# Performance work log

Hardware: AMD Instinct MI355X
Metric: run time of the kernel (lower is better)

The kernel has to match this reference:

```python
import jax, jax.numpy as jnp
import numpy as np
from jax import lax

K_NEIGHBORS = 50
KERNEL_DELTA = 1e-3


def _predict(x, w1, b1, w2, b2, w3, b3):
    # valuePredictor: Linear(512,256)-ELU-Linear(256,128)-ELU-Linear(128,5)
    h = jax.nn.elu(x @ w1 + b1)
    h = jax.nn.elu(h @ w2 + b2)
    p = h @ w3 + b3  # [B, 2 + action_space]
    value = p[:, 0]
    done = jax.nn.sigmoid(p[:, 1])
    logits = p[:, 2:]
    return value, done, logits


def _dnd_lookup(q, mem_keys, mem_vals, act):
    # q: [B, D]; mem_keys/mem_vals: [A, N, D]; act: [B] bank indices.
    # NEC-style DND: top-k nearest keys, inverse-distance kernel weighted value sum.
    B, D = q.shape
    A, N, _ = mem_keys.shape
    qn = jnp.sum(q * q, axis=-1)                      # [B]
    kn = jnp.sum(mem_keys * mem_keys, axis=-1)        # [A, N]
    dot = jnp.einsum('bd,and->ban', q, mem_keys)      # [B, A, N]
    dist = qn[:, None, None] + kn[None] - 2.0 * dot   # squared L2, [B, A, N]
    neg_d, idx = lax.top_k(-dist, K_NEIGHBORS)        # [B, A, K]
    d = -neg_d
    w = 1.0 / (d + KERNEL_DELTA)
    w = w / jnp.sum(w, axis=-1, keepdims=True)        # [B, A, K]
    vals_b = jnp.broadcast_to(mem_vals[None], (B, A, N, D))
    gathered = jnp.take_along_axis(vals_b, idx[..., None], axis=2)  # [B, A, K, D]
    out_all = jnp.sum(w[..., None] * gathered, axis=2)              # [B, A, D]
    return out_all[jnp.arange(B), act]                              # [B, D]


def setup_inputs() -> dict:
    key = jax.random.key(0)
    ks = jax.random.split(key, 8)
    B, D, A, N = 256, 512, 3, 25000
    x = jax.random.normal(ks[0], (B, D), dtype=jnp.float32)
    actions = jax.random.randint(ks[1], (B, 5), 0, A, dtype=jnp.int32)
    mem_keys = jax.random.normal(ks[2], (A, N, D), dtype=jnp.float32)
    mem_vals = jax.random.normal(ks[3], (A, N, D), dtype=jnp.float32)
    w1 = jax.random.normal(ks[4], (D, 256), dtype=jnp.float32) * (1.0 / np.sqrt(D))
    b1 = jnp.zeros((256,), jnp.float32)
    w2 = jax.random.normal(ks[5], (256, 128), dtype=jnp.float32) * (1.0 / np.sqrt(256))
    b2 = jnp.zeros((128,), jnp.float32)
    w3 = jax.random.normal(ks[6], (128, 5), dtype=jnp.float32) * (1.0 / np.sqrt(128))
    b3 = jnp.zeros((5,), jnp.float32)
    return {"x": x, "actions": actions, "mem_keys": mem_keys, "mem_vals": mem_vals,
            "w1": w1, "b1": b1, "w2": w2, "b2": b2, "w3": w3, "b3": b3}


def reference(x, actions, mem_keys, mem_vals, w1, b1, w2, b2, w3, b3):
    # Batched version of the per-sample loop: step-0 prediction on the
    # embedding, then 5 chained DND lookups each followed by a prediction.
    values, dones, logits = [], [], []
    v, dn, lg = _predict(x, w1, b1, w2, b2, w3, b3)
    values.append(v); dones.append(dn); logits.append(lg)
    emb = x
    for j in range(5):
        emb = _dnd_lookup(emb, mem_keys, mem_vals, actions[:, j])
        v, dn, lg = _predict(emb, w1, b1, w2, b2, w3, b3)
        values.append(v); dones.append(dn); logits.append(lg)
    values = jnp.stack(values, axis=1)   # [B, 6]
    dones = jnp.stack(dones, axis=1)     # [B, 6]
    logits = jnp.stack(logits, axis=1)   # [B, 6, 3]
    # pack into a single tensor [B, 6, 5]: (value, done, 3 action logits)
    return jnp.concatenate([values[..., None], dones[..., None], logits], axis=-1)
```

## Files before the change

### kernel.cpp

```cpp
#include <hip/hip_runtime.h>

#define BATCH 256
#define DIM 512
#define NACT 3
#define NMEM 25000
#define KNB 50
#define H1N 256
#define H2N 128
#define NSTEPS 5
#define KDELTA 0.001f

#define TB 128
#define TN 64
#define BK 64
#define NCH (DIM / BK)
#define NYT ((NMEM + TN - 1) / TN)

#define CAP 2048
#define MAXPT 12
#define ZTHR 2.40f

typedef __attribute__((ext_vector_type(8))) short short8;
typedef __attribute__((ext_vector_type(4))) float f32x4;

__device__ __forceinline__ unsigned short bf16rn(float f) {
    unsigned u = __float_as_uint(f);
    u += 0x7FFFu + ((u >> 16) & 1u);
    return (unsigned short)(u >> 16);
}
__device__ __forceinline__ float blo(unsigned u) { return __uint_as_float(u << 16); }
__device__ __forceinline__ float bhi(unsigned u) { return __uint_as_float(u & 0xFFFF0000u); }

__global__ __launch_bounds__(256)
void prep_keys_kernel(const float* __restrict__ rows, unsigned short* __restrict__ kb,
                      float* __restrict__ kn, int nrows) {
    int wave = threadIdx.x >> 6, lane = threadIdx.x & 63;
    int r = blockIdx.x * 4 + wave;
    if (r >= nrows) return;
    const float* p = rows + (size_t)r * DIM;
    float4 v0 = *(const float4*)(p + lane * 8);
    float4 v1 = *(const float4*)(p + lane * 8 + 4);
    float f[8] = {v0.x, v0.y, v0.z, v0.w, v1.x, v1.y, v1.z, v1.w};
    short8 hv;
    float s = 0.f;
    #pragma unroll
    for (int i = 0; i < 8; ++i) { hv[i] = (short)bf16rn(f[i]); s += f[i] * f[i]; }
    *(short8*)(kb + (size_t)r * DIM + lane * 8) = hv;
    for (int off = 32; off; off >>= 1) s += __shfl_down(s, off);
    if (lane == 0) kn[r] = s;
}

__global__ __launch_bounds__(256)
void knstats_kernel(const float* __restrict__ kn, float* __restrict__ knm,
                    float* __restrict__ knv) {
    int a = blockIdx.x, tid = threadIdx.x;
    __shared__ float ss[256], qq[256];
    float s = 0.f, q = 0.f;
    for (int i = tid; i < NMEM; i += 256) {
        float v = kn[a * NMEM + i];
        s += v; q += v * v;
    }
    ss[tid] = s; qq[tid] = q;
    __syncthreads();
    for (int st = 128; st > 0; st >>= 1) {
        if (tid < st) { ss[tid] += ss[tid + st]; qq[tid] += qq[tid + st]; }
        __syncthreads();
    }
    if (tid == 0) {
        float mean = ss[0] / (float)NMEM;
        knm[a] = mean;
        knv[a] = fmaxf(qq[0] / (float)NMEM - mean * mean, 0.f);
    }
}

__global__ __launch_bounds__(256)
void group_all_kernel(const int* __restrict__ actions,
                      int* __restrict__ perm, int* __restrict__ cnt) {
    int step = blockIdx.x;
    __shared__ int lcnt[NACT];
    __shared__ int lperm[NACT * BATCH];
    int tid = threadIdx.x;
    if (tid < NACT) lcnt[tid] = 0;
    __syncthreads();
    int a = actions[tid * NSTEPS + step];
    int pos = atomicAdd(&lcnt[a], 1);
    lperm[a * BATCH + pos] = tid;
    __syncthreads();
    if (tid < NACT) cnt[step * 4 + tid] = lcnt[tid];
    for (int aa = 0; aa < NACT; ++aa) {
        int c = lcnt[aa];
        int f = (c > 0) ? lperm[aa * BATCH] : 0;
        for (int i = c + tid; i < BATCH; i += 256) lperm[aa * BATCH + i] = f;
    }
    __syncthreads();
    for (int i = tid; i < NACT * BATCH; i += 256)
        perm[step * NACT * BATCH + i] = lperm[i];
}

__global__ __launch_bounds__(256)
void prep_predict_kernel(const float* __restrict__ x, unsigned short* __restrict__ eb,
                         float* __restrict__ qn, const int* __restrict__ actions,
                         const float* __restrict__ knm, const float* __restrict__ knv,
                         float* __restrict__ Tb, float* __restrict__ sw,
                         const float* __restrict__ w1, const float* __restrict__ b1,
                         const float* __restrict__ w2, const float* __restrict__ b2,
                         const float* __restrict__ w3, const float* __restrict__ b3,
                         float* __restrict__ out) {
    int b = blockIdx.x, tid = threadIdx.x;
    __shared__ float xs[DIM];
    __shared__ float red[256];
    __shared__ float h1[H1N];
    __shared__ float h2[H2N];
    float e0 = x[(size_t)b * DIM + tid];
    float e1 = x[(size_t)b * DIM + tid + 256];
    xs[tid] = e0; xs[tid + 256] = e1;
    eb[(size_t)b * DIM + tid] = bf16rn(e0);
    eb[(size_t)b * DIM + tid + 256] = bf16rn(e1);
    red[tid] = e0 * e0 + e1 * e1;
    __syncthreads();
    for (int s = 128; s > 0; s >>= 1) { if (tid < s) red[tid] += red[tid + s]; __syncthreads(); }
    if (tid == 0) {
        float q = red[0];
        qn[b] = q;
        int a0 = actions[b * NSTEPS];
        float s = sqrtf(knv[a0] + 4.f * q);
        Tb[b] = knm[a0] - ZTHR * s;
        sw[b] = s;
    }
    float acc = b1[tid];
    #pragma unroll 8
    for (int d = 0; d < DIM; ++d) acc = fmaf(xs[d], w1[d * H1N + tid], acc);
    h1[tid] = acc > 0.f ? acc : expm1f(acc);
    __syncthreads();
    if (tid < H2N) {
        float a2 = b2[tid];
        #pragma unroll 8
        for (int d = 0; d < H1N; ++d) a2 = fmaf(h1[d], w2[d * H2N + tid], a2);
        h2[tid] = a2 > 0.f ? a2 : expm1f(a2);
    }
    __syncthreads();
    if (tid < 5) {
        float p = b3[tid];
        for (int d = 0; d < H2N; ++d) p = fmaf(h2[d], w3[d * 5 + tid], p);
        float o = p;
        if (tid == 1) o = 1.0f / (1.0f + expf(-p));
        out[b * (6 * 5) + tid] = o;
    }
}

__global__ __launch_bounds__(256)
void dist_kernel(const unsigned short* __restrict__ eb, const unsigned short* __restrict__ kb,
                 const float* __restrict__ kn, const int* __restrict__ perm,
                 const int* __restrict__ cnt, const float* __restrict__ Tb,
                 unsigned* __restrict__ ccnt_t, unsigned short* __restrict__ candt) {
    int a = blockIdx.x;
    int c = cnt[a];
    int yt = blockIdx.y;
    int n0 = yt * TN;

    __shared__ __align__(16) unsigned short Qh[2][TB][BK];
    __shared__ __align__(16) unsigned short Kh[2][TN][BK];
    __shared__ int rows[TB];
    __shared__ float Tl[TB];
    __shared__ unsigned pcnt[TB];
    __shared__ unsigned short pids[TB][MAXPT];

    int tid = threadIdx.x;
    int lane = tid & 63, wave = tid >> 6;
    int wm = wave >> 1, wn = wave & 1;

    const int qr = tid >> 1, qc = (tid & 1) * 32, qswz = (qr & 7) * 8;
    const int kr = tid >> 2, kc = (tid & 3) * 16, kswz = (kr & 7) * 8;
    int krow = (n0 + kr < NMEM) ? (n0 + kr) : (NMEM - 1);
    const unsigned short* ksrc = kb + ((size_t)a * NMEM + krow) * DIM + kc;

    int nn[2]; float knv2[2]; bool nvalid[2];
    #pragma unroll
    for (int nf = 0; nf < 2; ++nf) {
        nn[nf] = n0 + wn * 32 + nf * 16 + (lane & 15);
        nvalid[nf] = nn[nf] < NMEM;
        knv2[nf] = nvalid[nf] ? kn[a * NMEM + nn[nf]] : 0.f;
    }

    for (int tb0 = 0; tb0 < c; tb0 += TB) {
        __syncthreads();
        if (tid < TB) {
            int i = tb0 + tid;
            int rr = perm[a * BATCH + (i < c ? i : 0)];
            rows[tid] = rr;
            Tl[tid] = Tb[rr];
            pcnt[tid] = 0;
        }
        __syncthreads();

        const int mlim = c - tb0;
        const unsigned short* qsrc = eb + (size_t)rows[qr] * DIM + qc;
        f32x4 acc[4][2] = {};
        short8 qA[4], qB[4], kA[2], kB[2];

        #pragma unroll
        for (int j = 0; j < 4; ++j) qA[j] = *(const short8*)(qsrc + j * 8);
        kA[0] = *(const short8*)(ksrc);
        kA[1] = *(const short8*)(ksrc + 8);
        #pragma unroll
        for (int j = 0; j < 4; ++j) qB[j] = *(const short8*)(qsrc + BK + j * 8);
        kB[0] = *(const short8*)(ksrc + BK);
        kB[1] = *(const short8*)(ksrc + BK + 8);
        #pragma unroll
        for (int j = 0; j < 4; ++j) *(short8*)&Qh[0][qr][(qc + j * 8) ^ qswz] = qA[j];
        *(short8*)&Kh[0][kr][(kc + 0) ^ kswz] = kA[0];
        *(short8*)&Kh[0][kr][(kc + 8) ^ kswz] = kA[1];
        __syncthreads();

        auto mfma_phase = [&](int B) {
            #pragma unroll
            for (int kk = 0; kk < BK; kk += 32) {
                int kcol = kk + (lane >> 4) * 8;
                short8 av[4], bv[2];
                #pragma unroll
                for (int nf = 0; nf < 2; ++nf) {
                    int n = wn * 32 + nf * 16 + (lane & 15);
                    bv[nf] = *(const short8*)&Kh[B][n][kcol ^ ((n & 7) * 8)];
                }
                #pragma unroll
                for (int mf = 0; mf < 4; ++mf) {
                    if (wm * 64 + mf * 16 < mlim) {
                        int m = wm * 64 + mf * 16 + (lane & 15);
                        av[mf] = *(const short8*)&Qh[B][m][kcol ^ ((m & 7) * 8)];
                        #pragma unroll
                        for (int nf = 0; nf < 2; ++nf)
                            acc[mf][nf] = __builtin_amdgcn_mfma_f32_16x16x32_bf16(av[mf], bv[nf], acc[mf][nf], 0, 0, 0);
                    }
                }
            }
        };

        #pragma unroll
        for (int p = 0; p < NCH / 2; ++p) {
            const int it = 2 * p;
            if (it + 2 < NCH) {
                const int d0 = (it + 2) * BK;
                #pragma unroll
                for (int j = 0; j < 4; ++j) qA[j] = *(const short8*)(qsrc + d0 + j * 8);
                kA[0] = *(const short8*)(ksrc + d0);
                kA[1] = *(const short8*)(ksrc + d0 + 8);
            }
            mfma_phase(0);
            {
                #pragma unroll
                for (int j = 0; j < 4; ++j) *(short8*)&Qh[1][qr][(qc + j * 8) ^ qswz] = qB[j];
                *(short8*)&Kh[1][kr][(kc + 0) ^ kswz] = kB[0];
                *(short8*)&Kh[1][kr][(kc + 8) ^ kswz] = kB[1];
                __syncthreads();
            }
            if (it + 3 < NCH) {
                const int d0 = (it + 3) * BK;
                #pragma unroll
                for (int j = 0; j < 4; ++j) qB[j] = *(const short8*)(qsrc + d0 + j * 8);
                kB[0] = *(const short8*)(ksrc + d0);
                kB[1] = *(const short8*)(ksrc + d0 + 8);
            }
            mfma_phase(1);
            if (it + 2 < NCH) {
                #pragma unroll
                for (int j = 0; j < 4; ++j) *(short8*)&Qh[0][qr][(qc + j * 8) ^ qswz] = qA[j];
                *(short8*)&Kh[0][kr][(kc + 0) ^ kswz] = kA[0];
                *(short8*)&Kh[0][kr][(kc + 8) ^ kswz] = kA[1];
                __syncthreads();
            }
        }

        #pragma unroll
        for (int mf = 0; mf < 4; ++mf) {
            if (wm * 64 + mf * 16 >= mlim) continue;
            #pragma unroll
            for (int r = 0; r < 4; ++r) {
                int m = wm * 64 + mf * 16 + (lane >> 4) * 4 + r;
                if (m >= mlim) continue;
                float Tv = Tl[m];
                #pragma unroll
                for (int nf = 0; nf < 2; ++nf) {
                    if (nvalid[nf]) {
                        float d = knv2[nf] - 2.0f * acc[mf][nf][r];
                        if (d < Tv) {
                            unsigned p = atomicAdd(&pcnt[m], 1u);
                            if (p < MAXPT) pids[m][p] = (unsigned short)nn[nf];
                        }
                    }
                }
            }
        }
        __syncthreads();
        if (tid < mlim) {
            int b = rows[tid];
            unsigned c0 = pcnt[tid];
            size_t slot = (size_t)b * NYT + yt;
            ccnt_t[slot] = c0;
            int w = c0 < MAXPT ? (int)c0 : MAXPT;
            for (int i = 0; i < w; ++i)
                candt[slot * MAXPT + i] = pids[tid][i];
        }
    }
}

__global__ __launch_bounds__(1024)
void selgp_kernel(const float* __restrict__ emb, const unsigned short* __restrict__ eb,
                  const unsigned short* __restrict__ kb,
                  const float* __restrict__ keys, const float* __restrict__ kn,
                  const float* __restrict__ qn,
                  const unsigned* __restrict__ ccnt_t, const unsigned short* __restrict__ candt,
                  const float* __restrict__ Tb_in, const float* __restrict__ sw_in,
                  const int* __restrict__ actions, int step,
                  const float* __restrict__ vals,
                  const float* __restrict__ knm, const float* __restrict__ knv,
                  float* __restrict__ emb_out, unsigned short* __restrict__ eb_out,
                  float* __restrict__ qn_out, float* __restrict__ Tb_out,
                  float* __restrict__ sw_out,
                  const float* __restrict__ w1, const float* __restrict__ b1,
                  const float* __restrict__ w2, const float* __restrict__ b2,
                  const float* __restrict__ w3, const float* __restrict__ b3,
                  float* __restrict__ out) {
    __shared__ float qs[DIM];
    __shared__ int tcnt[512];
    __shared__ int ovfS;
    __shared__ unsigned cntS;
    __shared__ int candb[CAP];
    __shared__ float dex[CAP];
    __shared__ float wsel[KNB];
    __shared__ int   isel[KNB];
    __shared__ float wsumS;
    __shared__ float part[1024];
    __shared__ float red[512];
    __shared__ float h1[H1N];
    __shared__ float h2[H2N];

    int b = blockIdx.x, tid = threadIdx.x;
    int a = actions[b * NSTEPS + step];

    if (tid < 128) *(float4*)&qs[tid * 4] = *(const float4*)(emb + (size_t)b * DIM + tid * 4);

    int own = 0;
    if (tid < 512) tcnt[tid] = 0;
    if (tid == 0) ovfS = 0;
    __syncthreads();
    if (tid < NYT) {
        unsigned c0 = ccnt_t[(size_t)b * NYT + tid];
        own = (c0 > MAXPT) ? MAXPT : (int)c0;
        tcnt[tid] = own;
        if (c0 > MAXPT) ovfS = 1;
    }
    __syncthreads();
    for (int off2 = 1; off2 < 512; off2 <<= 1) {
        int add = (tid < 512 && tid >= off2) ? tcnt[tid - off2] : 0;
        __syncthreads();
        if (tid < 512) tcnt[tid] += add;
        __syncthreads();
    }
    int C = tcnt[511];
    bool fb = (ovfS != 0) || (C < 128) || (C > CAP);
    if (!fb) {
        if (tid < NYT && own > 0) {
            int o = tcnt[tid] - own;
            size_t slot = (size_t)b * NYT + tid;
            for (int i = 0; i < own; ++i)
                candb[o + i] = (int)candt[slot * MAXPT + i];
        }
        __syncthreads();
    } else {
        float T = Tb_in[b], sd = sw_in[b];
        for (int it = 0; it < 10; ++it) {
            if (tid == 0) cntS = 0;
            __syncthreads();
            for (int n = tid; n < NMEM; n += 1024) {
                const unsigned short* kr = kb + ((size_t)a * NMEM + n) * DIM;
                float dot = 0.f;
                for (int dd = 0; dd < DIM; dd += 2) {
                    unsigned u = *(const unsigned*)(kr + dd);
                    dot = fmaf(blo(u), qs[dd], dot);
                    dot = fmaf(bhi(u), qs[dd + 1], dot);
                }
                float d = kn[a * NMEM + n] - 2.0f * dot;
                if (d < T) { unsigned p = atomicAdd(&cntS, 1u); if (p < CAP) candb[p] = n; }
            }
            __syncthreads();
            if (cntS >= 128 && cntS <= CAP) break;
            T += (cntS > CAP) ? -0.3f * sd : 0.6f * sd;
            __syncthreads();
        }
        C = (int)cntS; if (C > CAP) C = CAP;
    }

    float qnb = qn[b];
    const float* keysA = keys + (size_t)a * NMEM * DIM;
    {
        int cslot = tid >> 3, sub = tid & 7;
        int sweeps = (C + 127) >> 7;
        for (int sw = 0; sw < sweeps; ++sw) {
            int ci = sw * 128 + cslot;
            float dot = 0.f;
            int n = 0;
            if (ci < C) {
                n = candb[ci];
                const float* kr = keysA + (size_t)n * DIM;
                #pragma unroll
                for (int k = 0; k < 16; ++k) {
                    int o = sub * 4 + k * 32;
                    float4 kv = *(const float4*)(kr + o);
                    dot = fmaf(kv.x, qs[o+0], dot);
                    dot = fmaf(kv.y, qs[o+1], dot);
                    dot = fmaf(kv.z, qs[o+2], dot);
                    dot = fmaf(kv.w, qs[o+3], dot);
                }
            }
            dot += __shfl_xor(dot, 1);
            dot += __shfl_xor(dot, 2);
            dot += __shfl_xor(dot, 4);
            if (ci < C && sub == 0)
                dex[ci] = qnb + kn[a * NMEM + n] - 2.0f * dot;
        }
    }
    __syncthreads();

    for (int ci = tid; ci < C; ci += 1024) {
        float di = dex[ci]; int ni = candb[ci];
        int rank = 0;
        for (int j = 0; j < C; ++j) {
            float dj = dex[j];
            rank += (dj < di || (dj == di && candb[j] < ni)) ? 1 : 0;
        }
        if (rank < KNB) { wsel[rank] = 1.0f / (di + KDELTA); isel[rank] = ni; }
    }
    __syncthreads();
    if (tid == 0) {
        float ssum = 0.f;
        for (int i = 0; i < KNB; ++i) ssum += wsel[i];
        wsumS = ssum;
    }
    __syncthreads();
    if (tid < KNB) wsel[tid] = wsel[tid] / wsumS;
    __syncthreads();

    {
        int dim = tid & 511, h = tid >> 9;
        const float* va = vals + (size_t)a * NMEM * DIM + dim;
        float acc = 0.f;
        int k0 = h * 25;
        #pragma unroll 5
        for (int k = 0; k < 25; ++k)
            acc = fmaf(wsel[k0 + k], va[(size_t)isel[k0 + k] * DIM], acc);
        part[tid] = acc;
    }
    __syncthreads();
    if (tid < 512) {
        float e = part[tid] + part[tid + 512];
        emb_out[b * DIM + tid] = e;
        eb_out[b * DIM + tid] = bf16rn(e);
        qs[tid] = e;
        red[tid] = e * e;
    }
    __syncthreads();
    for (int s = 256; s > 0; s >>= 1) { if (tid < s) red[tid] += red[tid + s]; __syncthreads(); }
    if (tid == 0) {
        float q = red[0];
        qn_out[b] = q;
        if (step + 1 < NSTEPS) {
            int an = actions[b * NSTEPS + step + 1];
            float s = sqrtf(knv[an] + 4.f * q);
            Tb_out[b] = knm[an] - ZTHR * s;
            sw_out[b] = s;
        }
    }
    {
        int o = tid & (H1N - 1), q4 = tid >> 8;
        const float* wc = w1 + (size_t)q4 * 128 * H1N + o;
        const float* xc = qs + q4 * 128;
        float s = 0.f;
        #pragma unroll 8
        for (int d = 0; d < 128; ++d) s = fmaf(xc[d], wc[(size_t)d * H1N], s);
        part[tid] = s;
    }
    __syncthreads();
    if (tid < H1N) {
        float v = part[tid] + part[tid + H1N] + part[tid + 2 * H1N] + part[tid + 3 * H1N] + b1[tid];
        h1[tid] = v > 0.f ? v : expm1f(v);
    }
    __syncthreads();
    {
        int o = tid & (H2N - 1), q8 = tid >> 7;
        const float* wc = w2 + (size_t)q8 * 32 * H2N + o;
        const float* hc = h1 + q8 * 32;
        float s = 0.f;
        #pragma unroll 8
        for (int d = 0; d < 32; ++d) s = fmaf(hc[d], wc[(size_t)d * H2N], s);
        part[tid] = s;
    }
    __syncthreads();
    if (tid < H2N) {
        float v = b2[tid];
        #pragma unroll
        for (int q8 = 0; q8 < 8; ++q8) v += part[tid + q8 * H2N];
        h2[tid] = v > 0.f ? v : expm1f(v);
    }
    __syncthreads();
    if (tid < 5) {
        float p = b3[tid];
        for (int d = 0; d < H2N; ++d) p = fmaf(h2[d], w3[d * 5 + tid], p);
        float o = p;
        if (tid == 1) o = 1.0f / (1.0f + expf(-p));
        out[b * (6 * 5) + (step + 1) * 5 + tid] = o;
    }
}

extern "C" void kernel_launch(void* const* d_in, const int* in_sizes, int n_in,
                              void* d_out, int out_size, void* d_ws, size_t ws_size,
                              hipStream_t stream) {
    const float* x        = (const float*)d_in[0];
    const int*   actions  = (const int*)d_in[1];
    const float* mem_keys = (const float*)d_in[2];
    const float* mem_vals = (const float*)d_in[3];
    const float* w1 = (const float*)d_in[4];
    const float* b1 = (const float*)d_in[5];
    const float* w2 = (const float*)d_in[6];
    const float* b2 = (const float*)d_in[7];
    const float* w3 = (const float*)d_in[8];
    const float* b3 = (const float*)d_in[9];
    float* out = (float*)d_out;

    char* W = (char*)d_ws;
    unsigned short* kb    = (unsigned short*)W;
    unsigned short* eb    = (unsigned short*)(W + 76800000);
    float* kn    = (float*)(W + 77062144);
    float* qnb   = (float*)(W + 77362176);
    float* emb   = (float*)(W + 77363200);
    int*   perm  = (int*)(W + 77887488);
    int*   cntb  = (int*)(W + 77902848);
    float* knm   = (float*)(W + 77902976);
    float* knv   = (float*)(W + 77903104);
    float* Tb    = (float*)(W + 77903232);
    float* sw    = (float*)(W + 77904256);
    unsigned* ccnt_t       = (unsigned*)(W + 77905280);
    unsigned short* candt  = (unsigned short*)(W + 78305664);

    prep_keys_kernel<<<dim3((NACT * NMEM + 3) / 4), dim3(256), 0, stream>>>(mem_keys, kb, kn, NACT * NMEM);
    knstats_kernel<<<dim3(NACT), dim3(256), 0, stream>>>(kn, knm, knv);
    group_all_kernel<<<dim3(NSTEPS), dim3(256), 0, stream>>>(actions, perm, cntb);
    prep_predict_kernel<<<dim3(BATCH), dim3(256), 0, stream>>>(
        x, eb, qnb, actions, knm, knv, Tb, sw, w1, b1, w2, b2, w3, b3, out);

    const float* cur = x;
    for (int j = 0; j < NSTEPS; ++j) {
        dist_kernel<<<dim3(NACT, NYT), dim3(256), 0, stream>>>(
            eb, kb, kn, perm + j * NACT * BATCH, cntb + j * 4, Tb, ccnt_t, candt);
        selgp_kernel<<<dim3(BATCH), dim3(1024), 0, stream>>>(
            cur, eb, kb, mem_keys, kn, qnb, ccnt_t, candt, Tb, sw, actions, j, mem_vals,
            knm, knv, emb, eb, qnb, Tb, sw, w1, b1, w2, b2, w3, b3, out);
        cur = emb;
    }
}
```

Before: 446.8 us.

## Load MFMA operands directly from global memory, dropping LDS staging

```diff
diff --git a/kernel.cpp b/kernel.cpp
--- a/kernel.cpp
+++ b/kernel.cpp
@@ -12,8 +12,6 @@
 
 #define TB 128
 #define TN 64
-#define BK 64
-#define NCH (DIM / BK)
 #define NYT ((NMEM + TN - 1) / TN)
 
 #define CAP 2048
@@ -158,8 +156,6 @@
     int yt = blockIdx.y;
     int n0 = yt * TN;
 
-    __shared__ __align__(16) unsigned short Qh[2][TB][BK];
-    __shared__ __align__(16) unsigned short Kh[2][TN][BK];
     __shared__ int rows[TB];
     __shared__ float Tl[TB];
     __shared__ unsigned pcnt[TB];
@@ -168,18 +164,17 @@
     int tid = threadIdx.x;
     int lane = tid & 63, wave = tid >> 6;
     int wm = wave >> 1, wn = wave & 1;
-
-    const int qr = tid >> 1, qc = (tid & 1) * 32, qswz = (qr & 7) * 8;
-    const int kr = tid >> 2, kc = (tid & 3) * 16, kswz = (kr & 7) * 8;
-    int krow = (n0 + kr < NMEM) ? (n0 + kr) : (NMEM - 1);
-    const unsigned short* ksrc = kb + ((size_t)a * NMEM + krow) * DIM + kc;
+    int ksub = (lane >> 4) * 8;
 
     int nn[2]; float knv2[2]; bool nvalid[2];
+    const unsigned short* bsrc[2];
     #pragma unroll
     for (int nf = 0; nf < 2; ++nf) {
         nn[nf] = n0 + wn * 32 + nf * 16 + (lane & 15);
         nvalid[nf] = nn[nf] < NMEM;
+        int nr = nvalid[nf] ? nn[nf] : (NMEM - 1);
         knv2[nf] = nvalid[nf] ? kn[a * NMEM + nn[nf]] : 0.f;
+        bsrc[nf] = kb + ((size_t)a * NMEM + nr) * DIM + ksub;
     }
 
     for (int tb0 = 0; tb0 < c; tb0 += TB) {
@@ -194,85 +189,36 @@
         __syncthreads();
 
         const int mlim = c - tb0;
-        const unsigned short* qsrc = eb + (size_t)rows[qr] * DIM + qc;
+        const unsigned short* asrc[4];
+        bool afrag[4];
+        #pragma unroll
+        for (int mf = 0; mf < 4; ++mf) {
+            afrag[mf] = (wm * 64 + mf * 16) < mlim;
+            int m = wm * 64 + mf * 16 + (lane & 15);
+            asrc[mf] = eb + (size_t)rows[afrag[mf] ? m : 0] * DIM + ksub;
+        }
+
         f32x4 acc[4][2] = {};
-        short8 qA[4], qB[4], kA[2], kB[2];
-
         #pragma unroll
-        for (int j = 0; j < 4; ++j) qA[j] = *(const short8*)(qsrc + j * 8);
-        kA[0] = *(const short8*)(ksrc);
-        kA[1] = *(const short8*)(ksrc + 8);
-        #pragma unroll
-        for (int j = 0; j < 4; ++j) qB[j] = *(const short8*)(qsrc + BK + j * 8);
-        kB[0] = *(const short8*)(ksrc + BK);
-        kB[1] = *(const short8*)(ksrc + BK + 8);
-        #pragma unroll
-        for (int j = 0; j < 4; ++j) *(short8*)&Qh[0][qr][(qc + j * 8) ^ qswz] = qA[j];
-        *(short8*)&Kh[0][kr][(kc + 0) ^ kswz] = kA[0];
-        *(short8*)&Kh[0][kr][(kc + 8) ^ kswz] = kA[1];
-        __syncthreads();
-
-        auto mfma_phase = [&](int B) {
+        for (int kk = 0; kk < DIM; kk += 32) {
+            short8 bv[2];
             #pragma unroll
-            for (int kk = 0; kk < BK; kk += 32) {
-                int kcol = kk + (lane >> 4) * 8;
-                short8 av[4], bv[2];
-                #pragma unroll
-                for (int nf = 0; nf < 2; ++nf) {
-                    int n = wn * 32 + nf * 16 + (lane & 15);
-                    bv[nf] = *(const short8*)&Kh[B][n][kcol ^ ((n & 7) * 8)];
-                }
-                #pragma unroll
-                for (int mf = 0; mf < 4; ++mf) {
-                    if (wm * 64 + mf * 16 < mlim) {
-                        int m = wm * 64 + mf * 16 + (lane & 15);
-                        av[mf] = *(const short8*)&Qh[B][m][kcol ^ ((m & 7) * 8)];
-                        #pragma unroll
-                        for (int nf = 0; nf < 2; ++nf)
-                            acc[mf][nf] = __builtin_amdgcn_mfma_f32_16x16x32_bf16(av[mf], bv[nf], acc[mf][nf], 0, 0, 0);
-                    }
+            for (int nf = 0; nf < 2; ++nf)
+                bv[nf] = *(const short8*)(bsrc[nf] + kk);
+            #pragma unroll
+            for (int mf = 0; mf < 4; ++mf) {
+                if (afrag[mf]) {
+                    short8 av = *(const short8*)(asrc[mf] + kk);
+                    #pragma unroll
+                    for (int nf = 0; nf < 2; ++nf)
+                        acc[mf][nf] = __builtin_amdgcn_mfma_f32_16x16x32_bf16(av, bv[nf], acc[mf][nf], 0, 0, 0);
                 }
             }
-        };
-
-        #pragma unroll
-        for (int p = 0; p < NCH / 2; ++p) {
-            const int it = 2 * p;
-            if (it + 2 < NCH) {
-                const int d0 = (it + 2) * BK;
-                #pragma unroll
-                for (int j = 0; j < 4; ++j) qA[j] = *(const short8*)(qsrc + d0 + j * 8);
-                kA[0] = *(const short8*)(ksrc + d0);
-                kA[1] = *(const short8*)(ksrc + d0 + 8);
-            }
-            mfma_phase(0);
-            {
-                #pragma unroll
-                for (int j = 0; j < 4; ++j) *(short8*)&Qh[1][qr][(qc + j * 8) ^ qswz] = qB[j];
-                *(short8*)&Kh[1][kr][(kc + 0) ^ kswz] = kB[0];
-                *(short8*)&Kh[1][kr][(kc + 8) ^ kswz] = kB[1];
-                __syncthreads();
-            }
-            if (it + 3 < NCH) {
-                const int d0 = (it + 3) * BK;
-                #pragma unroll
-                for (int j = 0; j < 4; ++j) qB[j] = *(const short8*)(qsrc + d0 + j * 8);
-                kB[0] = *(const short8*)(ksrc + d0);
-                kB[1] = *(const short8*)(ksrc + d0 + 8);
-            }
-            mfma_phase(1);
-            if (it + 2 < NCH) {
-                #pragma unroll
-                for (int j = 0; j < 4; ++j) *(short8*)&Qh[0][qr][(qc + j * 8) ^ qswz] = qA[j];
-                *(short8*)&Kh[0][kr][(kc + 0) ^ kswz] = kA[0];
-                *(short8*)&Kh[0][kr][(kc + 8) ^ kswz] = kA[1];
-                __syncthreads();
-            }
         }
 
         #pragma unroll
         for (int mf = 0; mf < 4; ++mf) {
-            if (wm * 64 + mf * 16 >= mlim) continue;
+            if (!afrag[mf]) continue;
             #pragma unroll
             for (int r = 0; r < 4; ++r) {
                 int m = wm * 64 + mf * 16 + (lane >> 4) * 4 + r;
```

Result: slower. 628.1 us (+40.6%).
